# Optimization experiments

Measured on AMD Instinct MI355X. Metric: run time of the kernel, lower is better.

Reference implementation:

```python
import jax, jax.numpy as jnp
import numpy as np

EPS = 1e-5

def _normalize(v):
    # F.normalize(v, p=2, dim=-1, eps=1e-5): v / max(||v||_2, eps)
    n = jnp.sqrt(jnp.sum(v * v, axis=-1, keepdims=True))
    return v / jnp.maximum(n, EPS)

def setup_inputs() -> dict:
    key = jax.random.key(0)
    kx, ke = jax.random.split(key)
    B, T, C, K = 16, 2048, 512, 1024
    x = jax.random.normal(kx, (B, T, C), dtype=jnp.float32)
    emb = jax.random.normal(ke, (K, C), dtype=jnp.float32)  # embedding.weight
    return {"x": x, "emb": emb}

def reference(x, emb):
    B, T, C = x.shape
    # Squared distances (argmin of cdist == argmin of squared distance):
    x2 = jnp.sum(x * x, axis=-1, keepdims=True)          # [B,T,1]
    e2 = jnp.sum(emb * emb, axis=-1)                      # [K]
    xe = jnp.einsum('btc,kc->btk', x, emb)                # [B,T,K]
    dist2 = x2 - 2.0 * xe + e2                            # [B,T,K]
    idx = jnp.argmin(dist2, axis=-1)                      # [B,T] int
    quant = jnp.take(emb, idx, axis=0)                    # [B,T,C]
    x_norm = _normalize(x)
    q_norm = _normalize(quant)
    commitment_loss = jnp.mean((jax.lax.stop_gradient(q_norm) - x_norm) ** 2, axis=(1, 2))  # [B]
    codebook_loss = jnp.mean((q_norm - jax.lax.stop_gradient(x_norm)) ** 2, axis=(1, 2))    # [B]
    # Straight-through estimator
    quant_out = x + jax.lax.stop_gradient(quant - x)
    return quant_out, codebook_loss, commitment_loss, idx
```

## Files before the change

kernel.cpp:

```cpp
#include <hip/hip_runtime.h>

typedef unsigned short u16;
typedef unsigned int u32;
typedef _Float16 half8 __attribute__((ext_vector_type(8)));
typedef float f32x4 __attribute__((ext_vector_type(4)));

#define BT    32768
#define CD    512
#define KC    1024
#define LOFF1 16777216
#define LOFF2 16777232
#define IOFF  16777248

#define WS_EH   0
#define WS_E2   1048576
#define WS_PART 1052672

static __device__ __forceinline__ u16 f2h(float f) {
  union { _Float16 h; u16 u; } c;
  c.h = (_Float16)f;
  return c.u;
}

__global__ __launch_bounds__(256) void conve_kernel(const float* __restrict__ emb,
                                                    u16* __restrict__ eh,
                                                    float* __restrict__ e2) {
  const int lane = threadIdx.x & 63;
  const int r    = blockIdx.x * 4 + (threadIdx.x >> 6);
  const float4* er = reinterpret_cast<const float4*>(emb + (size_t)r * CD);
  const float4 a = er[lane*2], b = er[lane*2+1];
  uint4 o;
  o.x = (u32)f2h(a.x) | ((u32)f2h(a.y) << 16);
  o.y = (u32)f2h(a.z) | ((u32)f2h(a.w) << 16);
  o.z = (u32)f2h(b.x) | ((u32)f2h(b.y) << 16);
  o.w = (u32)f2h(b.z) | ((u32)f2h(b.w) << 16);
  reinterpret_cast<uint4*>(eh + (size_t)r * CD)[lane] = o;
  float s = a.x*a.x + a.y*a.y + a.z*a.z + a.w*a.w
          + b.x*b.x + b.y*b.y + b.z*b.z + b.w*b.w;
  for (int off = 32; off > 0; off >>= 1) s += __shfl_down(s, off, 64);
  if (lane == 0) e2[r] = s;
}

__global__ __launch_bounds__(256) void mfma_fused_kernel(
    const u16* __restrict__ eh, const float* __restrict__ e2,
    const float* __restrict__ x, const float* __restrict__ emb,
    float* __restrict__ out, float* __restrict__ part) {
  __shared__ __align__(16) char smem[70144];
  u16*    sA    = (u16*)smem;
  float*  e2s   = (float*)(smem + 65536);
  int*    win   = (int*)(smem + 69632);
  u32*    cand  = (u32*)smem;
  int*    top4k = (int*)(smem + 32768);
  double* dref  = (double*)(smem + 33792);
  float*  q2a   = (float*)(smem + 35840);
  float*  xqa   = (float*)(smem + 36864);
  float*  x2a   = (float*)(smem + 37888);

  const int tid  = threadIdx.x;
  const int wv   = tid >> 6;
  const int lane = tid & 63;
  const int lm   = lane & 15;
  const int lq   = lane >> 4;
  const int m0   = blockIdx.x * 64;

  {
    const float* xb = x + (size_t)m0 * CD;
    const int tl = tid & 15;
    const int tc = tid >> 4;
#pragma unroll 8
    for (int i = 0; i < 32; ++i) {
      const int r  = (i & 3) * 16 + tl;
      const int c4 = tc * 8 + (i >> 2);
      const float4 v = *(const float4*)(xb + (size_t)r * CD + c4 * 4);
      const int ks  = c4 >> 3;
      const int lqw = (c4 >> 1) & 3;
      const int j   = (c4 & 1) << 2;
      const int ti  = r >> 4, lmw = r & 15;
      uint2 o;
      o.x = (u32)f2h(v.x) | ((u32)f2h(v.y) << 16);
      o.y = (u32)f2h(v.z) | ((u32)f2h(v.w) << 16);
      *(uint2*)(sA + ((ti*16 + ks) << 9) + ((lqw << 4) + lmw) * 8 + j) = o;
    }
    e2s[tid]       = e2[tid];
    e2s[tid + 256] = e2[tid + 256];
    e2s[tid + 512] = e2[tid + 512];
    e2s[tid + 768] = e2[tid + 768];
  }
  __syncthreads();

  f32x4 acc[4][4];
#pragma unroll
  for (int i = 0; i < 4; ++i)
#pragma unroll
    for (int j = 0; j < 4; ++j)
      acc[i][j] = (f32x4){0.f, 0.f, 0.f, 0.f};

  u32 t0[16], t1[16];
#pragma unroll
  for (int s = 0; s < 16; ++s) { t0[s] = 0xFFFFFFFFu; t1[s] = 0xFFFFFFFFu; }

  const u16* eB = eh + (size_t)(wv*64 + lm) * CD + lq*8;

  half8 afA[4], afB[4], bfA[4], bfB[4];

#define PREF(IT, AF, BF) do {                                        \
    const int nt_ = (IT) >> 4, ks_ = (IT) & 15;                      \
    const u16* pb_ = eB + nt_ * 131072 + ks_ * 32;                   \
    BF[0] = *(const half8*)(pb_);                                    \
    BF[1] = *(const half8*)(pb_ + 8192);                             \
    BF[2] = *(const half8*)(pb_ + 16384);                            \
    BF[3] = *(const half8*)(pb_ + 24576);                            \
    const u16* pa_ = sA + ks_ * 512 + lane * 8;                      \
    AF[0] = *(const half8*)(pa_);                                    \
    AF[1] = *(const half8*)(pa_ + 8192);                             \
    AF[2] = *(const half8*)(pa_ + 16384);                            \
    AF[3] = *(const half8*)(pa_ + 24576);                            \
  } while (0)

#define MM(AF, BF) do {                                              \
    _Pragma("unroll") for (int ti_ = 0; ti_ < 4; ++ti_)              \
      _Pragma("unroll") for (int tj_ = 0; tj_ < 4; ++tj_)            \
        acc[ti_][tj_] = __builtin_amdgcn_mfma_f32_16x16x32_f16(      \
            AF[ti_], BF[tj_], acc[ti_][tj_], 0, 0, 0);               \
  } while (0)

#define FOLD(NT) do {                                                \
    _Pragma("unroll") for (int tj_ = 0; tj_ < 4; ++tj_) {            \
      const int col_ = (NT)*256 + wv*64 + tj_*16 + lm;               \
      const float ek_ = e2s[col_];                                   \
      _Pragma("unroll") for (int ti_ = 0; ti_ < 4; ++ti_)            \
        _Pragma("unroll") for (int rg_ = 0; rg_ < 4; ++rg_) {        \
          const float d_ = ek_ - 2.f * acc[ti_][tj_][rg_] + 1024.f;  \
          const u32 p_ = (__float_as_uint(d_) & 0xFFFFFC00u) | (u32)col_; \
          const int s_ = ti_*4 + rg_;                                \
          if (p_ < t0[s_]) { t1[s_] = t0[s_]; t0[s_] = p_; }         \
          else if (p_ < t1[s_]) { t1[s_] = p_; }                     \
          acc[ti_][tj_][rg_] = 0.f;                                  \
        }                                                            \
    }                                                                \
  } while (0)

  PREF(0, afA, bfA);
#pragma unroll 1
  for (int itp = 0; itp < 32; ++itp) {
    const int it = itp << 1;
    PREF(it + 1, afB, bfB);
    MM(afA, bfA);
    if (itp != 31) PREF(it + 2, afA, bfA);
    MM(afB, bfB);
    if ((itp & 7) == 7) FOLD(itp >> 3);
  }
#undef PREF
#undef MM
#undef FOLD

  __syncthreads();
#pragma unroll
  for (int s = 0; s < 16; ++s) {
    const int ti = s >> 2, reg = s & 3;
    const int row = ti*16 + lq*4 + reg;
    uint2 pr; pr.x = t0[s]; pr.y = t1[s];
    *reinterpret_cast<uint2*>(&cand[row*128 + wv*32 + lm*2]) = pr;
  }
  __syncthreads();

  if (tid < 64) {
    u32 u0 = 0xFFFFFFFFu, u1 = 0xFFFFFFFFu, u2 = 0xFFFFFFFFu, u3 = 0xFFFFFFFFu;
    for (int i = 0; i < 128; ++i) {
      const u32 v = cand[tid*128 + ((i + tid*2) & 127)];
      if (v < u3) {
        if (v < u2) {
          u3 = u2;
          if (v < u1) {
            u2 = u1;
            if (v < u0) { u1 = u0; u0 = v; } else { u1 = v; }
          } else { u2 = v; }
        } else { u3 = v; }
      }
    }
    top4k[tid*4+0] = (int)(u0 & 1023u);
    top4k[tid*4+1] = (int)(u1 & 1023u);
    top4k[tid*4+2] = (int)(u2 & 1023u);
    top4k[tid*4+3] = (int)(u3 & 1023u);
  }
  __syncthreads();

  {
    const int rr = tid >> 2, cc = tid & 3;
    const int k = top4k[rr*4 + cc];
    const float4* xr = reinterpret_cast<const float4*>(x   + (size_t)(m0+rr) * CD);
    const float4* er = reinterpret_cast<const float4*>(emb + (size_t)k * CD);
    double d0 = 0.0, d1 = 0.0;
    float q2 = 0.f, xq = 0.f, x2 = 0.f;
    for (int i = 0; i < CD/4; ++i) {
      const float4 a = xr[i], b = er[i];
      const double ta = (double)a.x - (double)b.x;
      const double tb = (double)a.y - (double)b.y;
      const double tc = (double)a.z - (double)b.z;
      const double td = (double)a.w - (double)b.w;
      d0 += ta*ta + tc*tc;
      d1 += tb*tb + td*td;
      q2 += b.x*b.x + b.y*b.y + b.z*b.z + b.w*b.w;
      xq += a.x*b.x + a.y*b.y + a.z*b.z + a.w*b.w;
      x2 += a.x*a.x + a.y*a.y + a.z*a.z + a.w*a.w;
    }
    dref[rr*4 + cc] = d0 + d1;
    q2a[rr*4 + cc] = q2;
    xqa[rr*4 + cc] = xq;
    if (cc == 0) x2a[rr] = x2;
  }
  __syncthreads();

  if (tid < 64) {
    double bd = dref[tid*4]; int bk = top4k[tid*4]; int bc = 0;
#pragma unroll
    for (int c = 1; c < 4; ++c) {
      const double dc = dref[tid*4 + c];
      const int kc = top4k[tid*4 + c];
      if (dc < bd || (dc == bd && kc < bk)) { bd = dc; bk = kc; bc = c; }
    }
    const int gr = m0 + tid;
    out[IOFF + gr] = (float)bk;
    win[tid] = bk;

    const float q2 = q2a[tid*4 + bc];
    const float xq = xqa[tid*4 + bc];
    const float x2 = x2a[tid];
    const float nx = fmaxf(sqrtf(x2), 1e-5f);
    const float nq = fmaxf(sqrtf(q2), 1e-5f);
    float s = q2/(nq*nq) + x2/(nx*nx) - 2.f*xq/(nx*nq);
    for (int off = 32; off > 0; off >>= 1) s += __shfl_down(s, off, 64);
    if (tid == 0) part[blockIdx.x] = s;
  }
  __syncthreads();

  {
    const float4* e4 = reinterpret_cast<const float4*>(emb);
    float4* ob = reinterpret_cast<float4*>(out + (size_t)m0 * CD);
#pragma unroll 8
    for (int i = 0; i < 32; ++i) {
      const int f = tid + (i << 8);
      const int k = win[f >> 7];
      ob[f] = e4[k*128 + (f & 127)];
    }
  }
}

__global__ void loss_write_kernel(const float* __restrict__ part,
                                  float* __restrict__ out) {
  const int t = threadIdx.x;
  if (t < 16) {
    float acc = 0.f;
    for (int i = 0; i < 32; ++i) acc += part[32*t + i];
    const float v = acc * (1.f / 1048576.f);
    out[LOFF1 + t] = v;
    out[LOFF2 + t] = v;
  }
}

extern "C" void kernel_launch(void* const* d_in, const int* in_sizes, int n_in,
                              void* d_out, int out_size, void* d_ws, size_t ws_size,
                              hipStream_t stream) {
  const float* x   = (const float*)d_in[0];
  const float* emb = (const float*)d_in[1];
  float* out = (float*)d_out;

  u16*   eh   = (u16*)((char*)d_ws + WS_EH);
  float* e2   = (float*)((char*)d_ws + WS_E2);
  float* part = (float*)((char*)d_ws + WS_PART);

  conve_kernel<<<KC / 4, 256, 0, stream>>>(emb, eh, e2);
  mfma_fused_kernel<<<BT / 64, 256, 0, stream>>>(eh, e2, x, emb, out, part);
  loss_write_kernel<<<1, 64, 0, stream>>>(part, out);
}
```

Before: 238.6 us.

## Pre-tile fp16 codebook for coalesced MFMA loads and deepen B prefetch ring

The codebook conversion kernel now writes the fp16 embedding in a tiled layout that matches the MFMA B-fragment order. Each wave's B load becomes one contiguous 1KB read instead of 16-byte pieces scattered across rows. The GEMM loop uses a 4-deep register ring for B fragments, issued before the x staging so they overlap it, and double-buffers the A fragments from LDS. It also raises wave priority around the MFMA burst and requests 2 blocks per CU through launch bounds. The deeper ring raises register pressure, and the final prefetches read past the codebook into the workspace without using the data.

Result: slower. 296.7 us (+24.4%).

```diff
diff --git a/kernel.cpp b/kernel.cpp
--- a/kernel.cpp
+++ b/kernel.cpp
@@ -34,14 +34,16 @@
   o.y = (u32)f2h(a.z) | ((u32)f2h(a.w) << 16);
   o.z = (u32)f2h(b.x) | ((u32)f2h(b.y) << 16);
   o.w = (u32)f2h(b.z) | ((u32)f2h(b.w) << 16);
-  reinterpret_cast<uint4*>(eh + (size_t)r * CD)[lane] = o;
+  const int gt = r >> 4, lm = r & 15;
+  const int ks = lane >> 2, lq = lane & 3;
+  reinterpret_cast<uint4*>(eh)[(gt*64 + ks*4 + lq)*16 + lm] = o;
   float s = a.x*a.x + a.y*a.y + a.z*a.z + a.w*a.w
           + b.x*b.x + b.y*b.y + b.z*b.z + b.w*b.w;
   for (int off = 32; off > 0; off >>= 1) s += __shfl_down(s, off, 64);
   if (lane == 0) e2[r] = s;
 }
 
-__global__ __launch_bounds__(256) void mfma_fused_kernel(
+__global__ __launch_bounds__(256, 2) void mfma_fused_kernel(
     const u16* __restrict__ eh, const float* __restrict__ e2,
     const float* __restrict__ x, const float* __restrict__ emb,
     float* __restrict__ out, float* __restrict__ part) {
@@ -62,6 +64,52 @@
   const int lm   = lane & 15;
   const int lq   = lane >> 4;
   const int m0   = blockIdx.x * 64;
+
+  const u16* eB = eh + wv*32768 + lane*8;
+
+  half8 af[2][4], bf[4][4];
+
+#define BLOAD(IT, BF) do {                                           \
+    const int nt_ = (IT) >> 4, ks_ = (IT) & 15;                      \
+    const u16* pb_ = eB + nt_ * 131072 + ks_ * 512;                  \
+    BF[0] = *(const half8*)(pb_);                                    \
+    BF[1] = *(const half8*)(pb_ + 8192);                             \
+    BF[2] = *(const half8*)(pb_ + 16384);                            \
+    BF[3] = *(const half8*)(pb_ + 24576);                            \
+  } while (0)
+
+#define ALOAD(IT, AF) do {                                           \
+    const u16* pa_ = sA + ((IT) & 15) * 512 + lane * 8;              \
+    AF[0] = *(const half8*)(pa_);                                    \
+    AF[1] = *(const half8*)(pa_ + 8192);                             \
+    AF[2] = *(const half8*)(pa_ + 16384);                            \
+    AF[3] = *(const half8*)(pa_ + 24576);                            \
+  } while (0)
+
+#define MM(AF, BF) do {                                              \
+    _Pragma("unroll") for (int ti_ = 0; ti_ < 4; ++ti_)              \
+      _Pragma("unroll") for (int tj_ = 0; tj_ < 4; ++tj_)            \
+        acc[ti_][tj_] = __builtin_amdgcn_mfma_f32_16x16x32_f16(      \
+            AF[ti_], BF[tj_], acc[ti_][tj_], 0, 0, 0);               \
+  } while (0)
+
+#define FOLD(NT) do {                                                \
+    _Pragma("unroll") for (int tj_ = 0; tj_ < 4; ++tj_) {            \
+      const int col_ = (NT)*256 + wv*64 + tj_*16 + lm;               \
+      const float ek_ = e2s[col_];                                   \
+      _Pragma("unroll") for (int ti_ = 0; ti_ < 4; ++ti_)            \
+        _Pragma("unroll") for (int rg_ = 0; rg_ < 4; ++rg_) {        \
+          const float d_ = ek_ - 2.f * acc[ti_][tj_][rg_] + 1024.f;  \
+          const u32 p_ = (__float_as_uint(d_) & 0xFFFFFC00u) | (u32)col_; \
+          const int s_ = ti_*4 + rg_;                                \
+          if (p_ < t0[s_]) { t1[s_] = t0[s_]; t0[s_] = p_; }         \
+          else if (p_ < t1[s_]) { t1[s_] = p_; }                     \
+          acc[ti_][tj_][rg_] = 0.f;                                  \
+        }                                                            \
+    }                                                                \
+  } while (0)
+
+  BLOAD(0, bf[0]); BLOAD(1, bf[1]); BLOAD(2, bf[2]); BLOAD(3, bf[3]);
 
   {
     const float* xb = x + (size_t)m0 * CD;
@@ -99,58 +147,23 @@
 #pragma unroll
   for (int s = 0; s < 16; ++s) { t0[s] = 0xFFFFFFFFu; t1[s] = 0xFFFFFFFFu; }
 
-  const u16* eB = eh + (size_t)(wv*64 + lm) * CD + lq*8;
-
-  half8 afA[4], afB[4], bfA[4], bfB[4];
-
-#define PREF(IT, AF, BF) do {                                        \
-    const int nt_ = (IT) >> 4, ks_ = (IT) & 15;                      \
-    const u16* pb_ = eB + nt_ * 131072 + ks_ * 32;                   \
-    BF[0] = *(const half8*)(pb_);                                    \
-    BF[1] = *(const half8*)(pb_ + 8192);                             \
-    BF[2] = *(const half8*)(pb_ + 16384);                            \
-    BF[3] = *(const half8*)(pb_ + 24576);                            \
-    const u16* pa_ = sA + ks_ * 512 + lane * 8;                      \
-    AF[0] = *(const half8*)(pa_);                                    \
-    AF[1] = *(const half8*)(pa_ + 8192);                             \
-    AF[2] = *(const half8*)(pa_ + 16384);                            \
-    AF[3] = *(const half8*)(pa_ + 24576);                            \
-  } while (0)
-
-#define MM(AF, BF) do {                                              \
-    _Pragma("unroll") for (int ti_ = 0; ti_ < 4; ++ti_)              \
-      _Pragma("unroll") for (int tj_ = 0; tj_ < 4; ++tj_)            \
-        acc[ti_][tj_] = __builtin_amdgcn_mfma_f32_16x16x32_f16(      \
-            AF[ti_], BF[tj_], acc[ti_][tj_], 0, 0, 0);               \
-  } while (0)
-
-#define FOLD(NT) do {                                                \
-    _Pragma("unroll") for (int tj_ = 0; tj_ < 4; ++tj_) {            \
-      const int col_ = (NT)*256 + wv*64 + tj_*16 + lm;               \
-      const float ek_ = e2s[col_];                                   \
-      _Pragma("unroll") for (int ti_ = 0; ti_ < 4; ++ti_)            \
-        _Pragma("unroll") for (int rg_ = 0; rg_ < 4; ++rg_) {        \
-          const float d_ = ek_ - 2.f * acc[ti_][tj_][rg_] + 1024.f;  \
-          const u32 p_ = (__float_as_uint(d_) & 0xFFFFFC00u) | (u32)col_; \
-          const int s_ = ti_*4 + rg_;                                \
-          if (p_ < t0[s_]) { t1[s_] = t0[s_]; t0[s_] = p_; }         \
-          else if (p_ < t1[s_]) { t1[s_] = p_; }                     \
-          acc[ti_][tj_][rg_] = 0.f;                                  \
-        }                                                            \
-    }                                                                \
-  } while (0)
-
-  PREF(0, afA, bfA);
+  ALOAD(0, af[0]);
+
 #pragma unroll 1
-  for (int itp = 0; itp < 32; ++itp) {
-    const int it = itp << 1;
-    PREF(it + 1, afB, bfB);
-    MM(afA, bfA);
-    if (itp != 31) PREF(it + 2, afA, bfA);
-    MM(afB, bfB);
-    if ((itp & 7) == 7) FOLD(itp >> 3);
-  }
-#undef PREF
+  for (int ob = 0; ob < 4; ++ob) {
+#pragma unroll
+    for (int b = 0; b < 16; ++b) {
+      const int it = ob * 16 + b;
+      ALOAD(it + 1, af[(b + 1) & 1]);
+      __builtin_amdgcn_s_setprio(1);
+      MM(af[b & 1], bf[b & 3]);
+      __builtin_amdgcn_s_setprio(0);
+      BLOAD(it + 4, bf[b & 3]);
+    }
+    FOLD(ob);
+  }
+#undef BLOAD
+#undef ALOAD
 #undef MM
 #undef FOLD
 
@@ -236,12 +249,12 @@
 
   {
     const float4* e4 = reinterpret_cast<const float4*>(emb);
-    float4* ob = reinterpret_cast<float4*>(out + (size_t)m0 * CD);
+    float4* ob4 = reinterpret_cast<float4*>(out + (size_t)m0 * CD);
 #pragma unroll 8
     for (int i = 0; i < 32; ++i) {
       const int f = tid + (i << 8);
       const int k = win[f >> 7];
-      ob[f] = e4[k*128 + (f & 127)];
+      ob4[f] = e4[k*128 + (f & 127)];
     }
   }
 }
```
